# Performance work log

Measured on AMD Instinct MI355X. Metric: run time of the kernel, lower is better.

## Reference

```python
import jax, jax.numpy as jnp
import numpy as np

N = 100000      # num nodes
E = 1600000     # num edges (avg degree 16)
H = 128         # hidden_channels
A = 8           # edge_attr_dim
HID = 16        # edge-MLP hidden dim
DELTA_T = 0.1
LN_EPS = 1e-5


def _layer_norm(x, g, b):
    mu = jnp.mean(x, axis=-1, keepdims=True)
    var = jnp.mean((x - mu) ** 2, axis=-1, keepdims=True)
    return (x - mu) * jax.lax.rsqrt(var + LN_EPS) * g + b


def _edge_mlp(ea, w1, b1, w2, b2):
    # [E,A] -> [E,1] -> [E]
    return (jnp.tanh(ea @ w1 + b1) @ w2 + b2).reshape(-1)


def _spmm_diff(vals, row, col, M, n):
    # Sparse matrix S = diag(d) + off, off[col,row] = vals (scatter-add on duplicates),
    # d = segment_sum(vals, col) with zeros replaced by 1.  Returns S @ M.
    d = jax.ops.segment_sum(vals, col, num_segments=n)
    d = d + (d == 0).astype(vals.dtype)
    off = jax.ops.segment_sum(vals[:, None] * M[row], col, num_segments=n)
    return d[:, None] * M + off


def setup_inputs() -> dict:
    key = jax.random.key(0)
    ks = jax.random.split(key, 12)
    def xavier(k, shape):
        lim = float(np.sqrt(6.0 / (shape[0] + shape[1])))
        return jax.random.uniform(k, shape, jnp.float32, -lim, lim)
    return {
        "u": jax.random.normal(ks[0], (N, H), jnp.float32),
        "edge_index": jax.random.randint(ks[1], (2, E), 0, N, jnp.int64),
        "edge_attr": jax.random.normal(ks[2], (E, A), jnp.float32),
        "num_nodes": N,
        "mlpx_w1": xavier(ks[3], (A, HID)), "mlpx_b1": jnp.zeros((HID,), jnp.float32),
        "mlpx_w2": xavier(ks[4], (HID, 1)), "mlpx_b2": jnp.zeros((1,), jnp.float32),
        "mlpz_w1": xavier(ks[5], (A, HID)), "mlpz_b1": jnp.zeros((HID,), jnp.float32),
        "mlpz_w2": xavier(ks[6], (HID, 1)), "mlpz_b2": jnp.zeros((1,), jnp.float32),
        "weight": xavier(ks[7], (H, H)),
        "az_weight": xavier(ks[8], (H, H)),
        "norm1_g": jnp.ones((H,), jnp.float32), "norm1_b": jnp.zeros((H,), jnp.float32),
        "norm2_g": jnp.ones((H,), jnp.float32), "norm2_b": jnp.zeros((H,), jnp.float32),
        "delta_g": jnp.float32(0.5),
    }


def reference(u, edge_index, edge_attr, num_nodes,
              mlpx_w1, mlpx_b1, mlpx_w2, mlpx_b2,
              mlpz_w1, mlpz_b1, mlpz_w2, mlpz_b2,
              weight, az_weight, norm1_g, norm1_b, norm2_g, norm2_b, delta_g):
    row, col = edge_index[0], edge_index[1]
    delta_x = _edge_mlp(edge_attr, mlpx_w1, mlpx_b1, mlpx_w2, mlpx_b2) + 1e-6
    delta_z = _edge_mlp(edge_attr, mlpz_w1, mlpz_b1, mlpz_w2, mlpz_b2) + 1e-6

    uw2 = (u @ weight) ** 2
    first = _spmm_diff(1.0 / delta_x, row, col, uw2, num_nodes)
    first = jax.nn.silu(_layer_norm(first, norm1_g, norm1_b))

    azt = _spmm_diff(delta_z, row, col, u, num_nodes) @ az_weight
    azt = jax.nn.silu(_layer_norm(azt, norm2_g, norm2_b)) + 1e-6

    u_next = u - DELTA_T * (first + delta_g * azt)
    return jnp.clip(u_next, -10.0, 10.0)
```

## Files before the change

### kernel.cpp

```cpp
#include <hip/hip_runtime.h>

#define HH 128
#define LN_EPS 1e-5f

typedef _Float16 f16x8 __attribute__((ext_vector_type(8)));
typedef _Float16 f16x4 __attribute__((ext_vector_type(4)));
typedef float f32x4 __attribute__((ext_vector_type(4)));

__device__ __forceinline__ ushort f2bf(float v) {
    unsigned u = __float_as_uint(v);
    unsigned r = (u + 0x7FFFu + ((u >> 16) & 1u)) >> 16;
    return (ushort)r;
}
__device__ __forceinline__ float bf2f(unsigned lo16) { return __uint_as_float(lo16 << 16); }

__device__ __forceinline__ bool detect_i64(const int* __restrict__ ei) {
    int odd = ei[2 * (threadIdx.x & 63) + 1];
    return __ballot(odd == 0) == ~0ULL;
}

__global__ __launch_bounds__(256) void k_hist_rank(
    const int* __restrict__ ei, int* __restrict__ cnt,
    ushort* __restrict__ rank, int E)
{
    bool f64 = detect_i64(ei);
    int e0 = (blockIdx.x * 256 + threadIdx.x) * 4;
    if (e0 >= E) return;
    int c[4];
    int nv = min(4, E - e0);
    if (f64) {
        if (nv == 4) {
            int4 a = *(const int4*)&ei[2 * ((size_t)E + e0)];
            int4 b = *(const int4*)&ei[2 * ((size_t)E + e0) + 4];
            c[0] = a.x; c[1] = a.z; c[2] = b.x; c[3] = b.z;
        } else {
            for (int i = 0; i < nv; ++i) c[i] = ei[2 * ((size_t)E + e0 + i)];
        }
    } else {
        if (nv == 4) {
            int4 a = *(const int4*)&ei[(size_t)E + e0];
            c[0] = a.x; c[1] = a.y; c[2] = a.z; c[3] = a.w;
        } else {
            for (int i = 0; i < nv; ++i) c[i] = ei[(size_t)E + e0 + i];
        }
    }
    ushort rk[4];
    for (int i = 0; i < nv; ++i) rk[i] = (ushort)atomicAdd(&cnt[c[i]], 1);
    if (nv == 4) {
        *(ushort4*)&rank[e0] = make_ushort4(rk[0], rk[1], rk[2], rk[3]);
    } else {
        for (int i = 0; i < nv; ++i) rank[e0 + i] = rk[i];
    }
}

__global__ __launch_bounds__(256) void k_scan_a(
    const int* __restrict__ cnt, int* __restrict__ off,
    int* __restrict__ bs, int N)
{
    __shared__ int sm[256];
    int tid = threadIdx.x;
    int base = blockIdx.x * 1024 + tid * 4;
    int v0 = base + 0 < N ? cnt[base + 0] : 0;
    int v1 = base + 1 < N ? cnt[base + 1] : 0;
    int v2 = base + 2 < N ? cnt[base + 2] : 0;
    int v3 = base + 3 < N ? cnt[base + 3] : 0;
    int s = v0 + v1 + v2 + v3;
    sm[tid] = s;
    __syncthreads();
    for (int o = 1; o < 256; o <<= 1) {
        int t = (tid >= o) ? sm[tid - o] : 0;
        __syncthreads();
        sm[tid] += t;
        __syncthreads();
    }
    int excl = sm[tid] - s;
    if (tid == 255) bs[blockIdx.x] = sm[tid];
    if (base + 0 < N) off[base + 0] = excl;
    if (base + 1 < N) off[base + 1] = excl + v0;
    if (base + 2 < N) off[base + 2] = excl + v0 + v1;
    if (base + 3 < N) off[base + 3] = excl + v0 + v1 + v2;
}

__global__ __launch_bounds__(256) void k_scan_bc(
    int* __restrict__ off, const int* __restrict__ bs,
    int N, int E, int nb)
{
    __shared__ int sm[256];
    int tid = threadIdx.x;
    int s = tid < nb ? bs[tid] : 0;
    sm[tid] = s;
    __syncthreads();
    for (int o = 1; o < 256; o <<= 1) {
        int t = (tid >= o) ? sm[tid - o] : 0;
        __syncthreads();
        sm[tid] += t;
        __syncthreads();
    }
    int incl = sm[tid];
    __syncthreads();
    sm[tid] = incl - s;
    __syncthreads();
    int i = blockIdx.x * 256 + tid;
    if (i < N) off[i] += sm[i >> 10];
    if (i == 0) off[N] = E;
}

__global__ __launch_bounds__(256) void k_mlp(
    const float* __restrict__ ea,
    const float* __restrict__ xw1, const float* __restrict__ xb1,
    const float* __restrict__ xw2, const float* __restrict__ xb2,
    const float* __restrict__ zw1, const float* __restrict__ zb1,
    const float* __restrict__ zw2, const float* __restrict__ zb2,
    unsigned* __restrict__ vxvz, int E)
{
    int lane = threadIdx.x & 63;
    int wid  = threadIdx.x >> 6;
    int lr = lane & 15, lg = lane >> 4;

    f16x8 wxh, wxl, wzh, wzl;
#pragma unroll
    for (int k = 0; k < 8; ++k) {
        float wx = xw1[k * 16 + lr];
        float wz = zw1[k * 16 + lr];
        _Float16 xh = (_Float16)wx, zh = (_Float16)wz;
        _Float16 xl = (_Float16)(wx - (float)xh);
        _Float16 zl = (_Float16)(wz - (float)zh);
        bool zz = (lg != 0);
        wxh[k] = zz ? (_Float16)0.f : xh;
        wxl[k] = zz ? (_Float16)0.f : xl;
        wzh[k] = zz ? (_Float16)0.f : zh;
        wzl[k] = zz ? (_Float16)0.f : zl;
    }
    float b1x[4], b1z[4], w2x[4], w2z[4];
#pragma unroll
    for (int r = 0; r < 4; ++r) {
        int j = lg * 4 + r;
        b1x[r] = xb1[j]; b1z[r] = zb1[j];
        w2x[r] = xw2[j]; w2z[r] = zw2[j];
    }
    float bx2 = xb2[0], bz2 = zb2[0];

    long long base = (long long)blockIdx.x * 256 + wid * 64;
    long long eL = base + lane;
    size_t eld = (size_t)(eL < (long long)E ? eL : (long long)E - 1);
    float4 a0 = *(const float4*)&ea[eld * 8];
    float4 a1 = *(const float4*)&ea[eld * 8 + 4];
    float aa[8] = {a0.x, a0.y, a0.z, a0.w, a1.x, a1.y, a1.z, a1.w};
    f16x8 ah, al;
#pragma unroll
    for (int i = 0; i < 8; ++i) {
        _Float16 h = (_Float16)aa[i];
        ah[i] = h;
        al[i] = (_Float16)(aa[i] - (float)h);
    }
    uint4 avh = *reinterpret_cast<uint4*>(&ah);
    uint4 avl = *reinterpret_cast<uint4*>(&al);

#pragma unroll
    for (int g = 0; g < 4; ++g) {
        int src = g * 16 + lr;
        uint4 bvh, bvl;
        bvh.x = (unsigned)__shfl((int)avh.x, src);
        bvh.y = (unsigned)__shfl((int)avh.y, src);
        bvh.z = (unsigned)__shfl((int)avh.z, src);
        bvh.w = (unsigned)__shfl((int)avh.w, src);
        bvl.x = (unsigned)__shfl((int)avl.x, src);
        bvl.y = (unsigned)__shfl((int)avl.y, src);
        bvl.z = (unsigned)__shfl((int)avl.z, src);
        bvl.w = (unsigned)__shfl((int)avl.w, src);
        if (lg != 0) {
            bvh.x = 0; bvh.y = 0; bvh.z = 0; bvh.w = 0;
            bvl.x = 0; bvl.y = 0; bvl.z = 0; bvl.w = 0;
        }
        f16x8 bh = *reinterpret_cast<f16x8*>(&bvh);
        f16x8 bl = *reinterpret_cast<f16x8*>(&bvl);

        f32x4 dx = (f32x4){0.f, 0.f, 0.f, 0.f};
        f32x4 dz = (f32x4){0.f, 0.f, 0.f, 0.f};
        dx = __builtin_amdgcn_mfma_f32_16x16x32_f16(wxh, bh, dx, 0, 0, 0);
        dx = __builtin_amdgcn_mfma_f32_16x16x32_f16(wxh, bl, dx, 0, 0, 0);
        dx = __builtin_amdgcn_mfma_f32_16x16x32_f16(wxl, bh, dx, 0, 0, 0);
        dz = __builtin_amdgcn_mfma_f32_16x16x32_f16(wzh, bh, dz, 0, 0, 0);
        dz = __builtin_amdgcn_mfma_f32_16x16x32_f16(wzh, bl, dz, 0, 0, 0);
        dz = __builtin_amdgcn_mfma_f32_16x16x32_f16(wzl, bh, dz, 0, 0, 0);

        float sx = 0.f, sz = 0.f;
#pragma unroll
        for (int r = 0; r < 4; ++r) {
            float tx = __expf(2.f * (dx[r] + b1x[r]));
            float tz = __expf(2.f * (dz[r] + b1z[r]));
            sx += __fdividef(tx - 1.f, tx + 1.f) * w2x[r];
            sz += __fdividef(tz - 1.f, tz + 1.f) * w2z[r];
        }
        sx += __shfl_xor(sx, 16); sx += __shfl_xor(sx, 32);
        sz += __shfl_xor(sz, 16); sz += __shfl_xor(sz, 32);

        long long e = base + g * 16 + lane;
        if (lane < 16 && e < (long long)E) {
            unsigned wx = f2bf(1.0f / (sx + bx2 + 1e-6f));
            unsigned wz = f2bf(sz + bz2 + 1e-6f);
            vxvz[e] = wx | (wz << 16);
        }
    }
}

__global__ __launch_bounds__(256) void k_fill(
    const int* __restrict__ ei, const int* __restrict__ off,
    const ushort* __restrict__ rank, const unsigned* __restrict__ vxvz,
    uint2* __restrict__ csr, int E)
{
    bool f64 = detect_i64(ei);
    int e0 = (blockIdx.x * 256 + threadIdx.x) * 4;
    if (e0 >= E) return;
    int nv = min(4, E - e0);
    int r[4], c[4];
    if (f64) {
        if (nv == 4) {
            int4 ra = *(const int4*)&ei[2 * (size_t)e0];
            int4 rb = *(const int4*)&ei[2 * (size_t)e0 + 4];
            int4 ca = *(const int4*)&ei[2 * ((size_t)E + e0)];
            int4 cb = *(const int4*)&ei[2 * ((size_t)E + e0) + 4];
            r[0] = ra.x; r[1] = ra.z; r[2] = rb.x; r[3] = rb.z;
            c[0] = ca.x; c[1] = ca.z; c[2] = cb.x; c[3] = cb.z;
        } else {
            for (int i = 0; i < nv; ++i) {
                r[i] = ei[2 * (size_t)(e0 + i)];
                c[i] = ei[2 * ((size_t)E + e0 + i)];
            }
        }
    } else {
        if (nv == 4) {
            int4 ra = *(const int4*)&ei[e0];
            int4 ca = *(const int4*)&ei[(size_t)E + e0];
            r[0] = ra.x; r[1] = ra.y; r[2] = ra.z; r[3] = ra.w;
            c[0] = ca.x; c[1] = ca.y; c[2] = ca.z; c[3] = ca.w;
        } else {
            for (int i = 0; i < nv; ++i) {
                r[i] = ei[e0 + i];
                c[i] = ei[(size_t)E + e0 + i];
            }
        }
    }
    ushort rk[4];
    unsigned wv[4];
    if (nv == 4) {
        ushort4 rr = *(const ushort4*)&rank[e0];
        rk[0] = rr.x; rk[1] = rr.y; rk[2] = rr.z; rk[3] = rr.w;
        uint4 vv = *(const uint4*)&vxvz[e0];
        wv[0] = vv.x; wv[1] = vv.y; wv[2] = vv.z; wv[3] = vv.w;
    } else {
        for (int i = 0; i < nv; ++i) { rk[i] = rank[e0 + i]; wv[i] = vxvz[e0 + i]; }
    }
    for (int i = 0; i < nv; ++i) {
        int p = off[c[i]] + rk[i];
        csr[p] = make_uint2((unsigned)r[i], wv[i]);
    }
}

#define WPITCH 136
__global__ __launch_bounds__(256) void k_gemm_fused(
    const float* __restrict__ A, const float* __restrict__ W0,
    const float* __restrict__ W1, _Float16* __restrict__ pk, int N)
{
    __shared__ _Float16 wt[256 * WPITCH];

    int tid = threadIdx.x;
    for (int it = 0; it < 8; ++it) {
        int tile = tid + it * 256;
        int k0 = (tile & 31) * 4, n0 = (tile >> 5) * 4;
        const float* src = (n0 < HH) ? W0 : W1;
        int cn = n0 & (HH - 1);
        float4 r0 = *(const float4*)&src[(k0 + 0) * HH + cn];
        float4 r1 = *(const float4*)&src[(k0 + 1) * HH + cn];
        float4 r2 = *(const float4*)&src[(k0 + 2) * HH + cn];
        float4 r3 = *(const float4*)&src[(k0 + 3) * HH + cn];
        const float* rr[4] = {(const float*)&r0, (const float*)&r1,
                              (const float*)&r2, (const float*)&r3};
#pragma unroll
        for (int j = 0; j < 4; ++j) {
            f16x4 v = {( _Float16)rr[0][j], (_Float16)rr[1][j],
                       ( _Float16)rr[2][j], (_Float16)rr[3][j]};
            *(f16x4*)&wt[(n0 + j) * WPITCH + k0] = v;
        }
    }
    __syncthreads();

    int w = tid >> 6, lane = tid & 63;
    int lr = lane & 15, lg = lane >> 4;

    f32x4 acc[2][16];
#pragma unroll
    for (int rt = 0; rt < 2; ++rt)
#pragma unroll
        for (int ct = 0; ct < 16; ++ct)
            acc[rt][ct] = (f32x4){0.f, 0.f, 0.f, 0.f};

    int rbase = blockIdx.x * 128 + w * 32 + lr;
    int ra0 = min(rbase,      N - 1);
    int ra1 = min(rbase + 16, N - 1);

    for (int ks = 0; ks < 4; ++ks) {
        int kofs = ks * 32 + lg * 8;
        f16x8 ufr[2];
#pragma unroll
        for (int rt = 0; rt < 2; ++rt) {
            const float* ap = &A[(size_t)(rt ? ra1 : ra0) * HH + kofs];
            float4 f0 = *(const float4*)ap;
            float4 f1 = *(const float4*)(ap + 4);
            f16x8 fr = {( _Float16)f0.x, (_Float16)f0.y, (_Float16)f0.z, (_Float16)f0.w,
                        ( _Float16)f1.x, (_Float16)f1.y, (_Float16)f1.z, (_Float16)f1.w};
            ufr[rt] = fr;
        }
#pragma unroll
        for (int ct = 0; ct < 16; ++ct) {
            f16x8 wfr = *(const f16x8*)&wt[(ct * 16 + lr) * WPITCH + kofs];
            acc[0][ct] = __builtin_amdgcn_mfma_f32_16x16x32_f16(wfr, ufr[0], acc[0][ct], 0, 0, 0);
            acc[1][ct] = __builtin_amdgcn_mfma_f32_16x16x32_f16(wfr, ufr[1], acc[1][ct], 0, 0, 0);
        }
    }

#pragma unroll
    for (int rt = 0; rt < 2; ++rt) {
        int r = blockIdx.x * 128 + w * 32 + rt * 16 + lr;
        if (r >= N) continue;
#pragma unroll
        for (int ct = 0; ct < 16; ++ct) {
            int c0 = ct * 16 + lg * 4;
            f16x4 o;
#pragma unroll
            for (int reg = 0; reg < 4; ++reg) {
                float v = acc[rt][ct][reg];
                if (ct < 8) v *= v;
                o[reg] = (_Float16)v;
            }
            *(f16x4*)&pk[(size_t)r * 256 + c0] = o;
        }
    }
}

__global__ __launch_bounds__(256) void k_gather(
    const uint2* __restrict__ csr, const int* __restrict__ off,
    const _Float16* __restrict__ pk, const float* __restrict__ u,
    const float* __restrict__ g1, const float* __restrict__ b1,
    const float* __restrict__ g2, const float* __restrict__ b2,
    const float* __restrict__ dgp, float* __restrict__ outp, int N)
{
    int wave = threadIdx.x >> 6, lane = threadIdx.x & 63;
    int node = blockIdx.x * 4 + wave;
    if (node >= N) return;
    int p = off[node], end = off[node + 1];

    const bool hi_edge = lane >= 32;
    const int  sub     = lane & 31;
    const bool is_az   = (lane & 16) != 0;

    float acc[8];
#pragma unroll
    for (int j = 0; j < 8; ++j) acc[j] = 0.f;
    float dv = 0.f;

    while (p + 3 < end) {
        uint2 ma0 = csr[p], ma1 = csr[p + 1];
        uint2 mb0 = csr[p + 2], mb1 = csr[p + 3];
        uint2 mA = hi_edge ? ma1 : ma0;
        uint2 mB = hi_edge ? mb1 : mb0;
        float wA = bf2f(is_az ? (mA.y >> 16) : (mA.y & 0xffffu));
        float wB = bf2f(is_az ? (mB.y >> 16) : (mB.y & 0xffffu));
        f16x8 qA = *(const f16x8*)&pk[(size_t)mA.x * 256 + sub * 8];
        f16x8 qB = *(const f16x8*)&pk[(size_t)mB.x * 256 + sub * 8];
#pragma unroll
        for (int j = 0; j < 8; ++j) acc[j] += wA * (float)qA[j];
#pragma unroll
        for (int j = 0; j < 8; ++j) acc[j] += wB * (float)qB[j];
        dv += wA + wB;
        p += 4;
    }
    while (p < end) {
        uint2 m0 = csr[p];
        uint2 m1 = (p + 1 < end) ? csr[p + 1] : m0;
        uint2 mm = hi_edge ? m1 : m0;
        float wv = bf2f(is_az ? (mm.y >> 16) : (mm.y & 0xffffu));
        if (hi_edge && p + 1 >= end) wv = 0.f;
        f16x8 q = *(const f16x8*)&pk[(size_t)mm.x * 256 + sub * 8];
#pragma unroll
        for (int j = 0; j < 8; ++j) acc[j] += wv * (float)q[j];
        dv += wv;
        p += 2;
    }

#pragma unroll
    for (int j = 0; j < 8; ++j) acc[j] += __shfl_xor(acc[j], 32);
    dv += __shfl_xor(dv, 32);
    if (dv == 0.f) dv = 1.f;

    f16x8 qc = *(const f16x8*)&pk[(size_t)node * 256 + sub * 8];
    float x[8];
#pragma unroll
    for (int j = 0; j < 8; ++j) x[j] = dv * (float)qc[j] + acc[j];

    float s = 0.f;
#pragma unroll
    for (int j = 0; j < 8; ++j) s += x[j];
    s += __shfl_xor(s, 1, 16); s += __shfl_xor(s, 2, 16);
    s += __shfl_xor(s, 4, 16); s += __shfl_xor(s, 8, 16);
    float mu = s * (1.f / 128.f);
    float s2 = 0.f;
#pragma unroll
    for (int j = 0; j < 8; ++j) { x[j] -= mu; s2 += x[j] * x[j]; }
    s2 += __shfl_xor(s2, 1, 16); s2 += __shfl_xor(s2, 2, 16);
    s2 += __shfl_xor(s2, 4, 16); s2 += __shfl_xor(s2, 8, 16);
    float rs = rsqrtf(s2 * (1.f / 128.f) + LN_EPS);

    int c8 = (sub & 15) * 8;
    const float* gp = is_az ? g2 : g1;
    const float* bp = is_az ? b2 : b1;
    float4 gv0 = *(const float4*)&gp[c8];
    float4 gv1 = *(const float4*)&gp[c8 + 4];
    float4 bv0 = *(const float4*)&bp[c8];
    float4 bv1 = *(const float4*)&bp[c8 + 4];
    float gA[8] = {gv0.x, gv0.y, gv0.z, gv0.w, gv1.x, gv1.y, gv1.z, gv1.w};
    float bA[8] = {bv0.x, bv0.y, bv0.z, bv0.w, bv1.x, bv1.y, bv1.z, bv1.w};

    float y[8];
#pragma unroll
    for (int j = 0; j < 8; ++j) {
        float v = x[j] * rs * gA[j] + bA[j];
        v = v / (1.f + __expf(-v));
        if (is_az) v += 1e-6f;
        y[j] = v;
    }

    float dg = *dgp;
    float yz[8];
#pragma unroll
    for (int j = 0; j < 8; ++j) yz[j] = __shfl_xor(y[j], 16);

    if (lane < 16) {
        size_t ub = (size_t)node * HH + c8;
        float4 u0 = *(const float4*)&u[ub];
        float4 u1 = *(const float4*)&u[ub + 4];
        float o[8];
        o[0] = u0.x; o[1] = u0.y; o[2] = u0.z; o[3] = u0.w;
        o[4] = u1.x; o[5] = u1.y; o[6] = u1.z; o[7] = u1.w;
#pragma unroll
        for (int j = 0; j < 8; ++j) {
            float v = o[j] - 0.1f * (y[j] + dg * yz[j]);
            o[j] = fminf(fmaxf(v, -10.f), 10.f);
        }
        *(float4*)&outp[ub]     = make_float4(o[0], o[1], o[2], o[3]);
        *(float4*)&outp[ub + 4] = make_float4(o[4], o[5], o[6], o[7]);
    }
}

extern "C" void kernel_launch(void* const* d_in, const int* in_sizes, int n_in,
                              void* d_out, int out_size, void* d_ws, size_t ws_size,
                              hipStream_t stream)
{
    const float* u   = (const float*)d_in[0];
    const int*   ei  = (const int*)d_in[1];
    const float* ea  = (const float*)d_in[2];
    const float* xw1 = (const float*)d_in[4];
    const float* xb1 = (const float*)d_in[5];
    const float* xw2 = (const float*)d_in[6];
    const float* xb2 = (const float*)d_in[7];
    const float* zw1 = (const float*)d_in[8];
    const float* zb1 = (const float*)d_in[9];
    const float* zw2 = (const float*)d_in[10];
    const float* zb2 = (const float*)d_in[11];
    const float* weight = (const float*)d_in[12];
    const float* azw = (const float*)d_in[13];
    const float* n1g = (const float*)d_in[14];
    const float* n1b = (const float*)d_in[15];
    const float* n2g = (const float*)d_in[16];
    const float* n2b = (const float*)d_in[17];
    const float* dgp = (const float*)d_in[18];

    int N = in_sizes[0] / HH;
    int E = in_sizes[2] / 8;

    _Float16* pk  = (_Float16*)d_ws;
    uint2* csr    = (uint2*)(pk + (size_t)N * 256);
    unsigned* vxvz= (unsigned*)(csr + E);
    ushort* rank  = (ushort*)(vxvz + E);
    int* cnt      = (int*)(rank + ((E + 1) & ~1));
    int* off      = cnt + N;
    int* bs       = off + N + 1;

    (void)hipMemsetAsync(cnt, 0, (size_t)N * sizeof(int), stream);

    k_mlp<<<(E + 255) / 256, 256, 0, stream>>>(
        ea, xw1, xb1, xw2, xb2, zw1, zb1, zw2, zb2, vxvz, E);

    k_hist_rank<<<(E / 4 + 255) / 256, 256, 0, stream>>>(ei, cnt, rank, E);

    int nb = (N + 1023) / 1024;
    k_scan_a<<<nb, 256, 0, stream>>>(cnt, off, bs, N);
    k_scan_bc<<<(N + 255) / 256, 256, 0, stream>>>(off, bs, N, E, nb);

    k_fill<<<(E / 4 + 255) / 256, 256, 0, stream>>>(ei, off, rank, vxvz, csr, E);

    k_gemm_fused<<<(N + 127) / 128, 256, 0, stream>>>(u, weight, azw, pk, N);

    k_gather<<<(N + 3) / 4, 256, 0, stream>>>(
        csr, off, pk, u, n1g, n1b, n2g, n2b, dgp, (float*)d_out, N);
}
```

Measured before the change: 325.1 us.

## Fuse edge MLP into CSR fill and store pre-shifted byte offsets

Merges the edge-MLP kernel with the CSR fill kernel, so edge weights are written straight into their CSR slot instead of going through an intermediate vxvz array. This removes one kernel launch and an E-sized write/read round trip. In exchange the MLP now runs after the scan and does scattered, unvectorized index loads, since only 16 lanes write per group. The gather kernel also reads precomputed byte offsets (row<<9) and indexes csr per lane, which trims address arithmetic and removes the select between two csr loads.

```diff
diff --git a/kernel.cpp b/kernel.cpp
--- a/kernel.cpp
+++ b/kernel.cpp
@@ -105,14 +105,16 @@
     if (i == 0) off[N] = E;
 }
 
-__global__ __launch_bounds__(256) void k_mlp(
+__global__ __launch_bounds__(256) void k_mlp_fill(
     const float* __restrict__ ea,
     const float* __restrict__ xw1, const float* __restrict__ xb1,
     const float* __restrict__ xw2, const float* __restrict__ xb2,
     const float* __restrict__ zw1, const float* __restrict__ zb1,
     const float* __restrict__ zw2, const float* __restrict__ zb2,
-    unsigned* __restrict__ vxvz, int E)
-{
+    const int* __restrict__ ei, const int* __restrict__ off,
+    const ushort* __restrict__ rank, uint2* __restrict__ csr, int E)
+{
+    bool f64 = detect_i64(ei);
     int lane = threadIdx.x & 63;
     int wid  = threadIdx.x >> 6;
     int lr = lane & 15, lg = lane >> 4;
@@ -197,63 +199,20 @@
 
         long long e = base + g * 16 + lane;
         if (lane < 16 && e < (long long)E) {
+            int ec = (int)e;
+            int r, c;
+            if (f64) {
+                r = ei[2 * (size_t)ec];
+                c = ei[2 * ((size_t)E + ec)];
+            } else {
+                r = ei[ec];
+                c = ei[(size_t)E + ec];
+            }
+            int p = off[c] + rank[ec];
             unsigned wx = f2bf(1.0f / (sx + bx2 + 1e-6f));
             unsigned wz = f2bf(sz + bz2 + 1e-6f);
-            vxvz[e] = wx | (wz << 16);
-        }
-    }
-}
-
-__global__ __launch_bounds__(256) void k_fill(
-    const int* __restrict__ ei, const int* __restrict__ off,
-    const ushort* __restrict__ rank, const unsigned* __restrict__ vxvz,
-    uint2* __restrict__ csr, int E)
-{
-    bool f64 = detect_i64(ei);
-    int e0 = (blockIdx.x * 256 + threadIdx.x) * 4;
-    if (e0 >= E) return;
-    int nv = min(4, E - e0);
-    int r[4], c[4];
-    if (f64) {
-        if (nv == 4) {
-            int4 ra = *(const int4*)&ei[2 * (size_t)e0];
-            int4 rb = *(const int4*)&ei[2 * (size_t)e0 + 4];
-            int4 ca = *(const int4*)&ei[2 * ((size_t)E + e0)];
-            int4 cb = *(const int4*)&ei[2 * ((size_t)E + e0) + 4];
-            r[0] = ra.x; r[1] = ra.z; r[2] = rb.x; r[3] = rb.z;
-            c[0] = ca.x; c[1] = ca.z; c[2] = cb.x; c[3] = cb.z;
-        } else {
-            for (int i = 0; i < nv; ++i) {
-                r[i] = ei[2 * (size_t)(e0 + i)];
-                c[i] = ei[2 * ((size_t)E + e0 + i)];
-            }
-        }
-    } else {
-        if (nv == 4) {
-            int4 ra = *(const int4*)&ei[e0];
-            int4 ca = *(const int4*)&ei[(size_t)E + e0];
-            r[0] = ra.x; r[1] = ra.y; r[2] = ra.z; r[3] = ra.w;
-            c[0] = ca.x; c[1] = ca.y; c[2] = ca.z; c[3] = ca.w;
-        } else {
-            for (int i = 0; i < nv; ++i) {
-                r[i] = ei[e0 + i];
-                c[i] = ei[(size_t)E + e0 + i];
-            }
-        }
-    }
-    ushort rk[4];
-    unsigned wv[4];
-    if (nv == 4) {
-        ushort4 rr = *(const ushort4*)&rank[e0];
-        rk[0] = rr.x; rk[1] = rr.y; rk[2] = rr.z; rk[3] = rr.w;
-        uint4 vv = *(const uint4*)&vxvz[e0];
-        wv[0] = vv.x; wv[1] = vv.y; wv[2] = vv.z; wv[3] = vv.w;
-    } else {
-        for (int i = 0; i < nv; ++i) { rk[i] = rank[e0 + i]; wv[i] = vxvz[e0 + i]; }
-    }
-    for (int i = 0; i < nv; ++i) {
-        int p = off[c[i]] + rk[i];
-        csr[p] = make_uint2((unsigned)r[i], wv[i]);
+            csr[p] = make_uint2((unsigned)r << 9, wx | (wz << 16));
+        }
     }
 }
 
@@ -350,9 +309,11 @@
     if (node >= N) return;
     int p = off[node], end = off[node + 1];
 
-    const bool hi_edge = lane >= 32;
-    const int  sub     = lane & 31;
-    const bool is_az   = (lane & 16) != 0;
+    const int  he   = lane >> 5;
+    const int  sub  = lane & 31;
+    const bool is_az = (lane & 16) != 0;
+    const unsigned sub16 = (unsigned)sub * 16;
+    const char* pkb = (const char*)pk;
 
     float acc[8];
 #pragma unroll
@@ -360,14 +321,12 @@
     float dv = 0.f;
 
     while (p + 3 < end) {
-        uint2 ma0 = csr[p], ma1 = csr[p + 1];
-        uint2 mb0 = csr[p + 2], mb1 = csr[p + 3];
-        uint2 mA = hi_edge ? ma1 : ma0;
-        uint2 mB = hi_edge ? mb1 : mb0;
+        uint2 mA = csr[p + he];
+        uint2 mB = csr[p + 2 + he];
         float wA = bf2f(is_az ? (mA.y >> 16) : (mA.y & 0xffffu));
         float wB = bf2f(is_az ? (mB.y >> 16) : (mB.y & 0xffffu));
-        f16x8 qA = *(const f16x8*)&pk[(size_t)mA.x * 256 + sub * 8];
-        f16x8 qB = *(const f16x8*)&pk[(size_t)mB.x * 256 + sub * 8];
+        f16x8 qA = *(const f16x8*)(pkb + mA.x + sub16);
+        f16x8 qB = *(const f16x8*)(pkb + mB.x + sub16);
 #pragma unroll
         for (int j = 0; j < 8; ++j) acc[j] += wA * (float)qA[j];
 #pragma unroll
@@ -376,12 +335,12 @@
         p += 4;
     }
     while (p < end) {
-        uint2 m0 = csr[p];
-        uint2 m1 = (p + 1 < end) ? csr[p + 1] : m0;
-        uint2 mm = hi_edge ? m1 : m0;
+        int idx = p + he;
+        bool ok = idx < end;
+        uint2 mm = csr[ok ? idx : p];
         float wv = bf2f(is_az ? (mm.y >> 16) : (mm.y & 0xffffu));
-        if (hi_edge && p + 1 >= end) wv = 0.f;
-        f16x8 q = *(const f16x8*)&pk[(size_t)mm.x * 256 + sub * 8];
+        if (!ok) wv = 0.f;
+        f16x8 q = *(const f16x8*)(pkb + mm.x + sub16);
 #pragma unroll
         for (int j = 0; j < 8; ++j) acc[j] += wv * (float)q[j];
         dv += wv;
@@ -393,7 +352,7 @@
     dv += __shfl_xor(dv, 32);
     if (dv == 0.f) dv = 1.f;
 
-    f16x8 qc = *(const f16x8*)&pk[(size_t)node * 256 + sub * 8];
+    f16x8 qc = *(const f16x8*)(pkb + ((unsigned)node << 9) + sub16);
     float x[8];
 #pragma unroll
     for (int j = 0; j < 8; ++j) x[j] = dv * (float)qc[j] + acc[j];
@@ -480,24 +439,21 @@
 
     _Float16* pk  = (_Float16*)d_ws;
     uint2* csr    = (uint2*)(pk + (size_t)N * 256);
-    unsigned* vxvz= (unsigned*)(csr + E);
-    ushort* rank  = (ushort*)(vxvz + E);
+    ushort* rank  = (ushort*)(csr + E);
     int* cnt      = (int*)(rank + ((E + 1) & ~1));
     int* off      = cnt + N;
     int* bs       = off + N + 1;
 
     (void)hipMemsetAsync(cnt, 0, (size_t)N * sizeof(int), stream);
 
-    k_mlp<<<(E + 255) / 256, 256, 0, stream>>>(
-        ea, xw1, xb1, xw2, xb2, zw1, zb1, zw2, zb2, vxvz, E);
-
     k_hist_rank<<<(E / 4 + 255) / 256, 256, 0, stream>>>(ei, cnt, rank, E);
 
     int nb = (N + 1023) / 1024;
     k_scan_a<<<nb, 256, 0, stream>>>(cnt, off, bs, N);
     k_scan_bc<<<(N + 255) / 256, 256, 0, stream>>>(off, bs, N, E, nb);
 
-    k_fill<<<(E / 4 + 255) / 256, 256, 0, stream>>>(ei, off, rank, vxvz, csr, E);
+    k_mlp_fill<<<(E + 255) / 256, 256, 0, stream>>>(
+        ea, xw1, xb1, xw2, xb2, zw1, zb1, zw2, zb2, ei, off, rank, csr, E);
 
     k_gemm_fused<<<(N + 127) / 128, 256, 0, stream>>>(u, weight, azw, pk, N);
 
```

Measured after the change: 304.2 us. 1.07x faster.
